# Kernel optimization log

Hardware: AMD Instinct MI355X
Metric: run time of the kernel (lower is better)

Reference implementation:

```python
import jax, jax.numpy as jnp
import numpy as np

N = 100_000        # nodes
E = 1_600_000      # edges (avg in-degree 16)
D_IN = 128
D_OUT = 128
K = 2              # hops


def setup_inputs() -> dict:
    key = jax.random.key(0)
    k1, k2, k3, k4 = jax.random.split(key, 4)
    feat = jax.random.normal(k1, (N, D_IN), dtype=jnp.float32)
    src = jax.random.randint(k2, (E,), 0, N, dtype=jnp.int64)
    # guarantee every node has in-degree >= 1 so deg**-0.5 is finite
    # (first N dst entries cover all nodes, rest random)
    dst_rand = jax.random.randint(k3, (E - N,), 0, N, dtype=jnp.int64)
    dst = jnp.concatenate([jnp.arange(N, dtype=jnp.int64), dst_rand])
    # xavier-normal-ish linear params: Linear(D_IN*(K+1) -> D_OUT)
    fan_in = D_IN * (K + 1)
    std = np.sqrt(2.0) * np.sqrt(2.0 / (fan_in + D_OUT))  # gain('relu') * xavier
    W = jax.random.normal(k4, (D_OUT, fan_in), dtype=jnp.float32) * std
    b = jnp.zeros((D_OUT,), dtype=jnp.float32)
    return {"feat": feat, "src": src, "dst": dst, "W": W, "b": b}


def reference(feat, src, dst, W, b):
    n = feat.shape[0]
    # in-degree based symmetric normalization: D^{-1/2} A D^{-1/2}
    deg = jax.ops.segment_sum(jnp.ones_like(dst, dtype=feat.dtype), dst,
                              num_segments=n)
    norm = (deg ** -0.5)[:, None]                 # [N, 1]
    fstack = [feat]
    h = feat
    for _ in range(K):
        h = h * norm                              # pre-scale by D^{-1/2}
        # SpMM: sum of source features into destination nodes
        h = jax.ops.segment_sum(h[src], dst, num_segments=n)
        h = h * norm                              # post-scale by D^{-1/2}
        fstack.append(h)
    x = jnp.concatenate(fstack, axis=-1)          # [N, D_IN*(K+1)]
    return x @ W.T + b
```

## Files before the change

### kernel.cpp

```cpp
#include <hip/hip_runtime.h>
#include <hip/hip_bf16.h>


#define D 128
#define TPB 256
#define GEMM_GRID 768

#define BSH 9
#define BSZ 512
#define NBMAX 256
#define EPT 16
#define CH (TPB * EPT)
#define LCAP 16384

typedef __attribute__((ext_vector_type(8))) short short8;
typedef __attribute__((ext_vector_type(4))) float f32x4;

__device__ __forceinline__ ushort f2bf(float f) {
    unsigned u = __float_as_uint(f);
    u += 0x7fff + ((u >> 16) & 1);
    return (ushort)(u >> 16);
}
__device__ __forceinline__ unsigned pack2bf(float x, float y) {
    return (unsigned)f2bf(x) | ((unsigned)f2bf(y) << 16);
}
__device__ __forceinline__ float bf_lo(unsigned v) { return __uint_as_float(v << 16); }
__device__ __forceinline__ float bf_hi(unsigned v) { return __uint_as_float(v & 0xffff0000u); }

__global__ __launch_bounds__(TPB) void count_kernel(
    const int* __restrict__ dst, int* __restrict__ bucketCnt, int e) {
    __shared__ int hist[NBMAX];
    int t = threadIdx.x;
    hist[t] = 0;
    __syncthreads();
    int base = blockIdx.x * CH;
    int lim = base + CH < e ? base + CH : e;
    for (int i = base + t; i < lim; i += TPB)
        atomicAdd(&hist[dst[i] >> BSH], 1);
    __syncthreads();
    int h = hist[t];
    if (h) atomicAdd(&bucketCnt[t], h);
}

__global__ __launch_bounds__(NBMAX) void bucket_scan_kernel(
    const int* __restrict__ bucketCnt, int* __restrict__ bucketBase, int nb, int e) {
    __shared__ int s[NBMAX];
    int t = threadIdx.x;
    int v = (t < nb) ? bucketCnt[t] : 0;
    s[t] = v;
    __syncthreads();
    for (int o = 1; o < NBMAX; o <<= 1) {
        int x = (t >= o) ? s[t - o] : 0;
        __syncthreads();
        s[t] += x;
        __syncthreads();
    }
    bucketBase[t] = s[t] - v;
    if (t == 0) bucketBase[nb] = e;
}

__global__ __launch_bounds__(TPB) void binscatter_kernel(
    const int* __restrict__ src, const int* __restrict__ dst,
    const int* __restrict__ bucketBase, int* __restrict__ gCursor,
    unsigned* __restrict__ tmp, int e) {
    __shared__ int hist[NBMAX];
    __shared__ int cellBase[NBMAX];
    int t = threadIdx.x;
    hist[t] = 0;
    __syncthreads();
    int base = blockIdx.x * CH;
    int b[EPT]; unsigned pk[EPT]; int r[EPT];
#pragma unroll
    for (int k = 0; k < EPT; ++k) {
        int i = base + k * TPB + t;
        b[k] = -1;
        if (i < e) {
            int d = dst[i];
            b[k] = d >> BSH;
            pk[k] = ((unsigned)src[i] << BSH) | (unsigned)(d & (BSZ - 1));
            r[k] = atomicAdd(&hist[b[k]], 1);
        }
    }
    __syncthreads();
    int h = hist[t];
    cellBase[t] = h ? bucketBase[t] + atomicAdd(&gCursor[t], h) : 0;
    __syncthreads();
#pragma unroll
    for (int k = 0; k < EPT; ++k)
        if (b[k] >= 0) tmp[cellBase[b[k]] + r[k]] = pk[k];
}

__global__ __launch_bounds__(TPB) void bucket_csr_kernel(
    const unsigned* __restrict__ tmp, const int* __restrict__ bucketBase,
    int* __restrict__ rs, float* __restrict__ norm, int* __restrict__ csr,
    int n, int e) {
    __shared__ int cnt[BSZ];
    __shared__ int off[BSZ];
    __shared__ int pr[TPB];
    __shared__ int lcsr[LCAP];
    int t = threadIdx.x;
    int bkt = blockIdx.x;
    int beg = bucketBase[bkt], end = bucketBase[bkt + 1];
    int m = end - beg;
    cnt[t] = 0; cnt[t + TPB] = 0;
    __syncthreads();
    for (int i = beg + t; i < end; i += TPB)
        atomicAdd(&cnt[tmp[i] & (BSZ - 1)], 1);
    __syncthreads();
    int c0 = cnt[2 * t], c1 = cnt[2 * t + 1];
    pr[t] = c0 + c1;
    int own = c0 + c1;
    __syncthreads();
    for (int o = 1; o < TPB; o <<= 1) {
        int x = (t >= o) ? pr[t - o] : 0;
        __syncthreads();
        pr[t] += x;
        __syncthreads();
    }
    int ex = pr[t] - own;
    off[2 * t] = ex;
    off[2 * t + 1] = ex + c0;
    __syncthreads();
    cnt[t] = 0; cnt[t + TPB] = 0;
    __syncthreads();
    for (int i = beg + t; i < end; i += TPB) {
        unsigned v = tmp[i];
        int l = v & (BSZ - 1);
        int r = atomicAdd(&cnt[l], 1);
        int idx = off[l] + r;
        if (idx < LCAP) lcsr[idx] = (int)(v >> BSH);
    }
    __syncthreads();
    int mm = m < LCAP ? m : LCAP;
    for (int i = t; i < mm; i += TPB) csr[beg + i] = lcsr[i];
    int node0 = bkt << BSH;
    for (int l = t; l < BSZ; l += TPB) {
        int node = node0 + l;
        if (node < n) {
            rs[node] = beg + off[l];
            norm[node] = rsqrtf((float)cnt[l]);
        } else if (node == n) {
            rs[n] = e;
        }
    }
}

__global__ __launch_bounds__(TPB) void prescale_kernel(
    const float* __restrict__ feat, unsigned* __restrict__ featb, int n) {
    int gid = blockIdx.x * TPB + threadIdx.x;
    int node = gid >> 6, c = gid & 63;
    if (node >= n) return;
    float2 f = ((const float2*)(feat + (size_t)node * D))[c];
    featb[(size_t)node * 64 + c] = pack2bf(f.x, f.y);
}

__global__ void wconv_kernel(const float* __restrict__ W, ushort* __restrict__ Wb, int n) {
    int i = blockIdx.x * TPB + threadIdx.x;
    if (i < n) Wb[i] = f2bf(W[i]);
}

__global__ __launch_bounds__(TPB) void spmm_kernel(
    const unsigned* __restrict__ hin, const int* __restrict__ rs,
    const int* __restrict__ csr, const float* __restrict__ norm,
    unsigned* __restrict__ hout, int n) {
    int w = (blockIdx.x * TPB + threadIdx.x) >> 6;
    if (w >= n) return;
    int lane = threadIdx.x & 63;
    int q = lane >> 4;
    int c = lane & 15;
    int beg = rs[w], end = rs[w + 1];
    float acc[8] = {};
#pragma unroll 4
    for (int j = beg + q; j < end; j += 4) {
        int u = csr[j];
        float s = norm[u];
        uint4 v = *(const uint4*)(hin + (size_t)u * 64 + c * 4);
        acc[0] = fmaf(s, bf_lo(v.x), acc[0]);
        acc[1] = fmaf(s, bf_hi(v.x), acc[1]);
        acc[2] = fmaf(s, bf_lo(v.y), acc[2]);
        acc[3] = fmaf(s, bf_hi(v.y), acc[3]);
        acc[4] = fmaf(s, bf_lo(v.z), acc[4]);
        acc[5] = fmaf(s, bf_hi(v.z), acc[5]);
        acc[6] = fmaf(s, bf_lo(v.w), acc[6]);
        acc[7] = fmaf(s, bf_hi(v.w), acc[7]);
    }
#pragma unroll
    for (int k = 0; k < 8; ++k) {
        acc[k] += __shfl_xor(acc[k], 16, 64);
        acc[k] += __shfl_xor(acc[k], 32, 64);
    }
    if (q == 0) {
        float nv = norm[w];
        uint4 r;
        r.x = pack2bf(acc[0] * nv, acc[1] * nv);
        r.y = pack2bf(acc[2] * nv, acc[3] * nv);
        r.z = pack2bf(acc[4] * nv, acc[5] * nv);
        r.w = pack2bf(acc[6] * nv, acc[7] * nv);
        *(uint4*)(hout + (size_t)w * 64 + c * 4) = r;
    }
}

__global__ __launch_bounds__(TPB) void gemm_mfma_kernel(
    const ushort* __restrict__ featb, const ushort* __restrict__ h1b,
    const ushort* __restrict__ h2b, const ushort* __restrict__ Wb,
    const float* __restrict__ bias, float* __restrict__ out, int n, int ntiles) {
    int lane = threadIdx.x & 63;
    int wave = threadIdx.x >> 6;
    int m = lane & 15, q = lane >> 4;

    short8 b[12][2];
#pragma unroll
    for (int ks = 0; ks < 12; ++ks)
#pragma unroll
        for (int t = 0; t < 2; ++t)
            b[ks][t] = *(const short8*)(Wb + (size_t)(wave * 32 + t * 16 + m) * 384
                                        + ks * 32 + q * 8);
    float bv0 = bias[wave * 32 + m];
    float bv1 = bias[wave * 32 + 16 + m];

    const ushort* srcs[3] = {featb, h1b, h2b};

    for (int tile = blockIdx.x; tile < ntiles; tile += gridDim.x) {
        int row = tile * 16 + m;
        bool va = row < n;
        size_t arow = (size_t)row * D;
        short8 a[12] = {};
        if (va) {
#pragma unroll
            for (int ks = 0; ks < 12; ++ks)
                a[ks] = *(const short8*)(srcs[ks >> 2] + arow + (ks & 3) * 32 + q * 8);
        }
        f32x4 acc0 = {}, acc1 = {};
#pragma unroll
        for (int ks = 0; ks < 12; ++ks) {
            acc0 = __builtin_amdgcn_mfma_f32_16x16x32_bf16(a[ks], b[ks][0], acc0, 0, 0, 0);
            acc1 = __builtin_amdgcn_mfma_f32_16x16x32_bf16(a[ks], b[ks][1], acc1, 0, 0, 0);
        }
        int r0 = tile * 16 + q * 4;
#pragma unroll
        for (int r = 0; r < 4; ++r) {
            int rw = r0 + r;
            if (rw < n) {
                size_t o = (size_t)rw * D + wave * 32 + m;
                out[o] = acc0[r] + bv0;
                out[o + 16] = acc1[r] + bv1;
            }
        }
    }
}

extern "C" void kernel_launch(void* const* d_in, const int* in_sizes, int n_in,
                              void* d_out, int out_size, void* d_ws, size_t ws_size,
                              hipStream_t stream) {
    const float* feat = (const float*)d_in[0];
    const int* src    = (const int*)d_in[1];
    const int* dst    = (const int*)d_in[2];
    const float* W    = (const float*)d_in[3];
    const float* bias = (const float*)d_in[4];
    float* out        = (float*)d_out;

    const int N = in_sizes[0] / D;
    const int E = in_sizes[1];
    const int NB = (N + BSZ - 1) >> BSH;

    char* ws = (char*)d_ws;
    size_t off = 0;
    auto bump = [&](size_t bytes) {
        char* p = ws + off;
        off += (bytes + 255) & ~(size_t)255;
        return p;
    };
    int* bucketCnt   = (int*)bump((size_t)2 * NBMAX * 4);
    int* gCursor     = bucketCnt + NBMAX;
    int* bucketBase  = (int*)bump((size_t)(NBMAX + 1) * 4);
    float* norm      = (float*)bump((size_t)N * 4);
    int* rs          = (int*)bump((size_t)(N + 1) * 4);
    unsigned* tmp    = (unsigned*)bump((size_t)E * 4);
    int* csr         = (int*)bump((size_t)E * 4);
    unsigned* featb  = (unsigned*)bump((size_t)N * 64 * 4);
    unsigned* h1b    = (unsigned*)bump((size_t)N * 64 * 4);
    unsigned* h2b    = (unsigned*)bump((size_t)N * 64 * 4);
    ushort* Wb       = (ushort*)bump((size_t)D * 384 * 2);
    (void)ws_size;

    hipMemsetAsync(bucketCnt, 0, (size_t)2 * NBMAX * 4, stream);

    const int nb_ch = (E + CH - 1) / CH;
    count_kernel<<<nb_ch, TPB, 0, stream>>>(dst, bucketCnt, E);
    bucket_scan_kernel<<<1, NBMAX, 0, stream>>>(bucketCnt, bucketBase, NB, E);
    binscatter_kernel<<<nb_ch, TPB, 0, stream>>>(src, dst, bucketBase, gCursor, tmp, E);
    bucket_csr_kernel<<<NB, TPB, 0, stream>>>(tmp, bucketBase, rs, norm, csr, N, E);

    const int pres_blocks = (N * 64 + TPB - 1) / TPB;
    prescale_kernel<<<pres_blocks, TPB, 0, stream>>>(feat, featb, N);
    wconv_kernel<<<(D * 384 + TPB - 1) / TPB, TPB, 0, stream>>>(W, Wb, D * 384);

    const int spmm_blocks = (N * 64 + TPB - 1) / TPB;
    spmm_kernel<<<spmm_blocks, TPB, 0, stream>>>(featb, rs, csr, norm, h1b, N);
    spmm_kernel<<<spmm_blocks, TPB, 0, stream>>>(h1b, rs, csr, norm, h2b, N);

    const int ntiles = (N + 15) / 16;
    gemm_mfma_kernel<<<GEMM_GRID, TPB, 0, stream>>>(
        (const ushort*)featb, (const ushort*)h1b, (const ushort*)h2b,
        Wb, bias, out, N, ntiles);
}
```

Baseline: 331.7 us.

## Fuse preprocessing kernels and use fixed-capacity buckets to drop count/scan pass

Replaces the count, scan and binscatter sequence with a single scatter into fixed-capacity per-bucket slots, using the per-bucket cursor as the count. Fuses bf16 feature conversion and weight conversion into the same launch as the scatter. Row starts are stored with degrees as int2, so SpMM no longer reads rs[w+1]. This removes a full pass over dst and several launches. In exchange, it assumes no bucket exceeds LCAP edges and enlarges the tmp and csr buffers.

Result: faster. 308.8 us (-6.9%).

```diff
diff --git a/kernel.cpp b/kernel.cpp
--- a/kernel.cpp
+++ b/kernel.cpp
@@ -27,89 +27,76 @@
 __device__ __forceinline__ float bf_lo(unsigned v) { return __uint_as_float(v << 16); }
 __device__ __forceinline__ float bf_hi(unsigned v) { return __uint_as_float(v & 0xffff0000u); }
 
-__global__ __launch_bounds__(TPB) void count_kernel(
-    const int* __restrict__ dst, int* __restrict__ bucketCnt, int e) {
-    __shared__ int hist[NBMAX];
-    int t = threadIdx.x;
-    hist[t] = 0;
-    __syncthreads();
-    int base = blockIdx.x * CH;
-    int lim = base + CH < e ? base + CH : e;
-    for (int i = base + t; i < lim; i += TPB)
-        atomicAdd(&hist[dst[i] >> BSH], 1);
-    __syncthreads();
-    int h = hist[t];
-    if (h) atomicAdd(&bucketCnt[t], h);
-}
-
-__global__ __launch_bounds__(NBMAX) void bucket_scan_kernel(
-    const int* __restrict__ bucketCnt, int* __restrict__ bucketBase, int nb, int e) {
-    __shared__ int s[NBMAX];
-    int t = threadIdx.x;
-    int v = (t < nb) ? bucketCnt[t] : 0;
-    s[t] = v;
-    __syncthreads();
-    for (int o = 1; o < NBMAX; o <<= 1) {
-        int x = (t >= o) ? s[t - o] : 0;
-        __syncthreads();
-        s[t] += x;
-        __syncthreads();
-    }
-    bucketBase[t] = s[t] - v;
-    if (t == 0) bucketBase[nb] = e;
-}
-
-__global__ __launch_bounds__(TPB) void binscatter_kernel(
+__global__ __launch_bounds__(TPB) void mega_kernel(
     const int* __restrict__ src, const int* __restrict__ dst,
-    const int* __restrict__ bucketBase, int* __restrict__ gCursor,
-    unsigned* __restrict__ tmp, int e) {
+    int* __restrict__ gCursor, unsigned* __restrict__ tmp,
+    const float* __restrict__ feat, unsigned* __restrict__ featb,
+    const float* __restrict__ W, ushort* __restrict__ Wb,
+    int e, int n, int nbin, int npre) {
     __shared__ int hist[NBMAX];
     __shared__ int cellBase[NBMAX];
     int t = threadIdx.x;
-    hist[t] = 0;
-    __syncthreads();
-    int base = blockIdx.x * CH;
-    int b[EPT]; unsigned pk[EPT]; int r[EPT];
-#pragma unroll
-    for (int k = 0; k < EPT; ++k) {
-        int i = base + k * TPB + t;
-        b[k] = -1;
-        if (i < e) {
-            int d = dst[i];
-            b[k] = d >> BSH;
-            pk[k] = ((unsigned)src[i] << BSH) | (unsigned)(d & (BSZ - 1));
-            r[k] = atomicAdd(&hist[b[k]], 1);
-        }
-    }
-    __syncthreads();
-    int h = hist[t];
-    cellBase[t] = h ? bucketBase[t] + atomicAdd(&gCursor[t], h) : 0;
-    __syncthreads();
-#pragma unroll
-    for (int k = 0; k < EPT; ++k)
-        if (b[k] >= 0) tmp[cellBase[b[k]] + r[k]] = pk[k];
+    int bid = blockIdx.x;
+
+    if (bid < nbin) {
+        hist[t] = 0;
+        __syncthreads();
+        int base = bid * CH;
+        int b[EPT]; unsigned pk[EPT]; int r[EPT];
+#pragma unroll
+        for (int k = 0; k < EPT; ++k) {
+            int i = base + k * TPB + t;
+            b[k] = -1;
+            if (i < e) {
+                int d = dst[i];
+                b[k] = d >> BSH;
+                pk[k] = ((unsigned)src[i] << BSH) | (unsigned)(d & (BSZ - 1));
+                r[k] = atomicAdd(&hist[b[k]], 1);
+            }
+        }
+        __syncthreads();
+        int h = hist[t];
+        cellBase[t] = h ? t * LCAP + atomicAdd(&gCursor[t], h) : 0;
+        __syncthreads();
+#pragma unroll
+        for (int k = 0; k < EPT; ++k)
+            if (b[k] >= 0) tmp[cellBase[b[k]] + r[k]] = pk[k];
+    } else if (bid < nbin + npre) {
+        int gid = (bid - nbin) * TPB + t;
+        int node = gid >> 6, c = gid & 63;
+        if (node >= n) return;
+        float2 f = ((const float2*)(feat + (size_t)node * D))[c];
+        featb[(size_t)node * 64 + c] = pack2bf(f.x, f.y);
+    } else {
+        int i = ((bid - nbin - npre) * TPB + t) * 4;
+        float4 w = *(const float4*)(W + i);
+        ushort4 o;
+        o.x = f2bf(w.x); o.y = f2bf(w.y); o.z = f2bf(w.z); o.w = f2bf(w.w);
+        *(ushort4*)(Wb + i) = o;
+    }
 }
 
 __global__ __launch_bounds__(TPB) void bucket_csr_kernel(
-    const unsigned* __restrict__ tmp, const int* __restrict__ bucketBase,
-    int* __restrict__ rs, float* __restrict__ norm, int* __restrict__ csr,
-    int n, int e) {
+    const unsigned* __restrict__ tmp, const int* __restrict__ gCursor,
+    int2* __restrict__ rsdeg, float* __restrict__ norm, int* __restrict__ csr,
+    int n) {
     __shared__ int cnt[BSZ];
     __shared__ int off[BSZ];
     __shared__ int pr[TPB];
     __shared__ int lcsr[LCAP];
     int t = threadIdx.x;
     int bkt = blockIdx.x;
-    int beg = bucketBase[bkt], end = bucketBase[bkt + 1];
-    int m = end - beg;
+    int beg = bkt * LCAP;
+    int m = gCursor[bkt];
+    int end = beg + m;
     cnt[t] = 0; cnt[t + TPB] = 0;
     __syncthreads();
     for (int i = beg + t; i < end; i += TPB)
         atomicAdd(&cnt[tmp[i] & (BSZ - 1)], 1);
     __syncthreads();
     int c0 = cnt[2 * t], c1 = cnt[2 * t + 1];
-    pr[t] = c0 + c1;
     int own = c0 + c1;
+    pr[t] = own;
     __syncthreads();
     for (int o = 1; o < TPB; o <<= 1) {
         int x = (t >= o) ? pr[t - o] : 0;
@@ -137,30 +124,14 @@
     for (int l = t; l < BSZ; l += TPB) {
         int node = node0 + l;
         if (node < n) {
-            rs[node] = beg + off[l];
+            rsdeg[node] = make_int2(beg + off[l], cnt[l]);
             norm[node] = rsqrtf((float)cnt[l]);
-        } else if (node == n) {
-            rs[n] = e;
-        }
-    }
-}
-
-__global__ __launch_bounds__(TPB) void prescale_kernel(
-    const float* __restrict__ feat, unsigned* __restrict__ featb, int n) {
-    int gid = blockIdx.x * TPB + threadIdx.x;
-    int node = gid >> 6, c = gid & 63;
-    if (node >= n) return;
-    float2 f = ((const float2*)(feat + (size_t)node * D))[c];
-    featb[(size_t)node * 64 + c] = pack2bf(f.x, f.y);
-}
-
-__global__ void wconv_kernel(const float* __restrict__ W, ushort* __restrict__ Wb, int n) {
-    int i = blockIdx.x * TPB + threadIdx.x;
-    if (i < n) Wb[i] = f2bf(W[i]);
+        }
+    }
 }
 
 __global__ __launch_bounds__(TPB) void spmm_kernel(
-    const unsigned* __restrict__ hin, const int* __restrict__ rs,
+    const uint4* __restrict__ hin4, const int2* __restrict__ rsdeg,
     const int* __restrict__ csr, const float* __restrict__ norm,
     unsigned* __restrict__ hout, int n) {
     int w = (blockIdx.x * TPB + threadIdx.x) >> 6;
@@ -168,13 +139,14 @@
     int lane = threadIdx.x & 63;
     int q = lane >> 4;
     int c = lane & 15;
-    int beg = rs[w], end = rs[w + 1];
+    int2 rd = rsdeg[w];
+    int beg = rd.x, end = rd.x + rd.y;
     float acc[8] = {};
 #pragma unroll 4
     for (int j = beg + q; j < end; j += 4) {
         int u = csr[j];
         float s = norm[u];
-        uint4 v = *(const uint4*)(hin + (size_t)u * 64 + c * 4);
+        uint4 v = hin4[(u << 4) + c];
         acc[0] = fmaf(s, bf_lo(v.x), acc[0]);
         acc[1] = fmaf(s, bf_hi(v.x), acc[1]);
         acc[2] = fmaf(s, bf_lo(v.y), acc[2]);
@@ -270,34 +242,30 @@
         off += (bytes + 255) & ~(size_t)255;
         return p;
     };
-    int* bucketCnt   = (int*)bump((size_t)2 * NBMAX * 4);
-    int* gCursor     = bucketCnt + NBMAX;
-    int* bucketBase  = (int*)bump((size_t)(NBMAX + 1) * 4);
+    int* gCursor     = (int*)bump((size_t)NBMAX * 4);
     float* norm      = (float*)bump((size_t)N * 4);
-    int* rs          = (int*)bump((size_t)(N + 1) * 4);
-    unsigned* tmp    = (unsigned*)bump((size_t)E * 4);
-    int* csr         = (int*)bump((size_t)E * 4);
+    int2* rsdeg      = (int2*)bump((size_t)N * 8);
+    unsigned* tmp    = (unsigned*)bump((size_t)NB * LCAP * 4);
+    int* csr         = (int*)bump((size_t)NB * LCAP * 4);
     unsigned* featb  = (unsigned*)bump((size_t)N * 64 * 4);
     unsigned* h1b    = (unsigned*)bump((size_t)N * 64 * 4);
     unsigned* h2b    = (unsigned*)bump((size_t)N * 64 * 4);
     ushort* Wb       = (ushort*)bump((size_t)D * 384 * 2);
     (void)ws_size;
 
-    hipMemsetAsync(bucketCnt, 0, (size_t)2 * NBMAX * 4, stream);
-
-    const int nb_ch = (E + CH - 1) / CH;
-    count_kernel<<<nb_ch, TPB, 0, stream>>>(dst, bucketCnt, E);
-    bucket_scan_kernel<<<1, NBMAX, 0, stream>>>(bucketCnt, bucketBase, NB, E);
-    binscatter_kernel<<<nb_ch, TPB, 0, stream>>>(src, dst, bucketBase, gCursor, tmp, E);
-    bucket_csr_kernel<<<NB, TPB, 0, stream>>>(tmp, bucketBase, rs, norm, csr, N, E);
-
-    const int pres_blocks = (N * 64 + TPB - 1) / TPB;
-    prescale_kernel<<<pres_blocks, TPB, 0, stream>>>(feat, featb, N);
-    wconv_kernel<<<(D * 384 + TPB - 1) / TPB, TPB, 0, stream>>>(W, Wb, D * 384);
+    hipMemsetAsync(gCursor, 0, (size_t)NBMAX * 4, stream);
+
+    const int nbin = (E + CH - 1) / CH;
+    const int npre = (N * 64 + TPB - 1) / TPB;
+    const int nwcv = (D * 384 / 4 + TPB - 1) / TPB;
+    mega_kernel<<<nbin + npre + nwcv, TPB, 0, stream>>>(
+        src, dst, gCursor, tmp, feat, featb, W, Wb, E, N, nbin, npre);
+
+    bucket_csr_kernel<<<NB, TPB, 0, stream>>>(tmp, gCursor, rsdeg, norm, csr, N);
 
     const int spmm_blocks = (N * 64 + TPB - 1) / TPB;
-    spmm_kernel<<<spmm_blocks, TPB, 0, stream>>>(featb, rs, csr, norm, h1b, N);
-    spmm_kernel<<<spmm_blocks, TPB, 0, stream>>>(h1b, rs, csr, norm, h2b, N);
+    spmm_kernel<<<spmm_blocks, TPB, 0, stream>>>((const uint4*)featb, rsdeg, csr, norm, h1b, N);
+    spmm_kernel<<<spmm_blocks, TPB, 0, stream>>>((const uint4*)h1b, rsdeg, csr, norm, h2b, N);
 
     const int ntiles = (N + 15) / 16;
     gemm_mfma_kernel<<<GEMM_GRID, TPB, 0, stream>>>(
```
